# Kernel optimization log

Hardware: AMD Instinct MI355X
Metric: run time of the kernel (lower is better)

## Reference

```python
import jax, jax.numpy as jnp
import numpy as np

H = 16          # N_heads (Attention default)
DH = 32         # d per head (Attention default)
EPS = 1e-5      # torch LayerNorm eps
SCALE = float(1.0 / np.sqrt(DH))


def _ln(z, w, b):
    # LayerNorm over the last TWO dims (normalized_shape=(N_x, channel)), affine w/b of shape [2S, C]
    m = jnp.mean(z, axis=(-2, -1), keepdims=True)
    v = jnp.mean(jnp.square(z - m), axis=(-2, -1), keepdims=True)
    return (z - m) * jax.lax.rsqrt(v + EPS) * w + b


def _attention(a, p):
    # a: [2S, C]. Faithful to source: y = x.clone(), scores are NOT softmaxed (causal_mask=False).
    lx_w, lx_b, ly_w, ly_b, lf_w, lf_b, wq_w, wq_b, wk_w, wk_b, wv_w, wv_b, w1, b1, w2, b2, w3, b3 = p
    L = a.shape[0]
    xn = _ln(a, lx_w, lx_b)
    yn = _ln(a, ly_w, ly_b)
    q = (xn @ wq_w.T + wq_b).reshape(L, H, DH).transpose(1, 0, 2)  # [H, 2S, d]
    k = (yn @ wk_w.T + wk_b).reshape(L, H, DH).transpose(1, 0, 2)
    v = (yn @ wv_w.T + wv_b).reshape(L, H, DH).transpose(1, 0, 2)
    scores = jnp.einsum('hqd,hkd->hqk', q, k) * SCALE               # no softmax in source
    o = jnp.einsum('hqk,hkd->hqd', scores, v).transpose(1, 0, 2).reshape(L, H * DH)
    x1 = a + o @ w1.T + b1
    h = jax.nn.gelu(_ln(x1, lf_w, lf_b) @ w2.T + b2, approximate=False)
    return x1 + h @ w3.T + b3


def _forward(x, params):
    # x: [3, S, S, C]; params are stacked over the idx axis [S, ...] (one Attention per idx, shared across modes)
    S = x.shape[1]
    attn = jax.vmap(_attention, in_axes=(0, 0))
    for m1, m2 in [(0, 1), (2, 0), (1, 2)]:
        a = jnp.concatenate([x[m1], jnp.swapaxes(x[m2], 0, 1)], axis=1)  # [S, 2S, C]
        c = attn(a, params)                                              # [S, 2S, C]
        x = x.at[m1].set(c[:, :S, :])
        x = x.at[m2].set(c[:, S:, :])
    return x


def setup_inputs() -> dict:
    S, C, W = 16, 1024, 4
    D = H * DH   # 512
    L = 2 * S    # 32
    key = jax.random.key(0)
    ks = jax.random.split(key, 8)
    rn = lambda k, shp, s: jax.random.normal(k, shp, dtype=jnp.float32) * s
    return {
        'x': rn(ks[0], (3, S, S, C), 1.0),
        'lx_w': jnp.ones((S, L, C), jnp.float32), 'lx_b': jnp.zeros((S, L, C), jnp.float32),
        'ly_w': jnp.ones((S, L, C), jnp.float32), 'ly_b': jnp.zeros((S, L, C), jnp.float32),
        'lf_w': jnp.ones((S, L, C), jnp.float32), 'lf_b': jnp.zeros((S, L, C), jnp.float32),
        'wq_w': rn(ks[1], (S, D, C), 0.02), 'wq_b': jnp.zeros((S, D), jnp.float32),
        'wk_w': rn(ks[2], (S, D, C), 0.02), 'wk_b': jnp.zeros((S, D), jnp.float32),
        'wv_w': rn(ks[3], (S, D, C), 0.02), 'wv_b': jnp.zeros((S, D), jnp.float32),
        'w1': rn(ks[4], (S, C, D), 0.02), 'b1': jnp.zeros((S, C), jnp.float32),
        'w2': rn(ks[5], (S, W * C, C), 0.02), 'b2': jnp.zeros((S, W * C), jnp.float32),
        'w3': rn(ks[6], (S, C, W * C), 0.02), 'b3': jnp.zeros((S, C), jnp.float32),
    }


def reference(x, lx_w, lx_b, ly_w, ly_b, lf_w, lf_b, wq_w, wq_b, wk_w, wk_b, wv_w, wv_b, w1, b1, w2, b2, w3, b3):
    params = (lx_w, lx_b, ly_w, ly_b, lf_w, lf_b, wq_w, wq_b, wk_w, wk_b, wv_w, wv_b, w1, b1, w2, b2, w3, b3)
    return _forward(x, params)
```

## Files before the change

kernel.cpp:

```cpp
#include <hip/hip_runtime.h>


#define C1024 1024
#define D512  512
#define FF4096 4096
#define NELEM 32768.0f
#define EPSLN 1e-5f
#define QSCALE 0.17677669529663687f
#define LP 258

typedef __attribute__((ext_vector_type(8))) short bf16x8;
typedef __attribute__((ext_vector_type(4))) float f32x4;
typedef unsigned short u16;

__device__ inline u16 f2bf(float f) {
    unsigned u = __float_as_uint(f);
    u += 0x7fffu + ((u >> 16) & 1u);
    return (u16)(u >> 16);
}

__device__ inline bf16x8 cvt8(f32x4 a, f32x4 b) {
    bf16x8 r;
    r[0] = (short)f2bf(a[0]); r[1] = (short)f2bf(a[1]);
    r[2] = (short)f2bf(a[2]); r[3] = (short)f2bf(a[3]);
    r[4] = (short)f2bf(b[0]); r[5] = (short)f2bf(b[1]);
    r[6] = (short)f2bf(b[2]); r[7] = (short)f2bf(b[3]);
    return r;
}

struct Cvt6 {
    const float* s[6];
    u16* d[6];
    int N32[6], kzs[6], base[6];
};
__global__ void __launch_bounds__(256, 8) k_cvt6(Cvt6 a) {
    __shared__ float lds[16 * LP];
    int bid = blockIdx.x;
    int ts = 0;
#pragma unroll
    for (int j = 1; j < 6; ++j) if (bid >= a.base[j]) ts = j;
    int local = bid - a.base[ts];
    int kzs = a.kzs[ts], N32 = a.N32[ts];
    int kz = local % kzs;
    int b  = (local / kzs) & 1;
    int nt = (local / (kzs * 2)) % N32;
    int i  = local / (kzs * 2 * N32);
    int K = kzs * 256;
    int t = threadIdx.x;
    int row = t >> 4, c16 = t & 15;
    const float* Sp = a.s[ts] + ((size_t)((i * N32 + nt) * 32) + b * 16 + row) * K + kz * 256 + c16 * 4;
    float* Lrow = lds + row * LP + c16 * 4;
#pragma unroll
    for (int j = 0; j < 4; ++j) {
        f32x4 v = *(const f32x4*)(Sp + 64 * j);
        Lrow[64 * j]     = v[0];
        Lrow[64 * j + 1] = v[1];
        Lrow[64 * j + 2] = v[2];
        Lrow[64 * j + 3] = v[3];
    }
    __syncthreads();
    u16* Dp = a.d[ts] + (((size_t)(i * N32 + nt) * (kzs * 8) + kz * 8) * 1024) + b * 512;
#pragma unroll
    for (int p = 0; p < 2; ++p) {
        int u = p * 2048 + t * 8;
        int c   = u >> 9;
        int rem = u & 511;
        int kg = rem >> 7;
        int lr = (rem >> 3) & 15;
        const float* src = lds + lr * LP + c * 32 + kg * 8;
        f32x4 lo, hi;
        lo[0] = src[0]; lo[1] = src[1]; lo[2] = src[2]; lo[3] = src[3];
        hi[0] = src[4]; hi[1] = src[5]; hi[2] = src[6]; hi[3] = src[7];
        *(bf16x8*)(Dp + c * 1024 + rem) = cvt8(lo, hi);
    }
}

__device__ inline void mmz(const u16* __restrict__ act, const u16* __restrict__ p,
                           int nkk, f32x4& acc0, f32x4& acc1) {
#pragma unroll 4
    for (int j = 0; j < nkk; ++j) {
        bf16x8 aF = *(const bf16x8*)(act + j * 32);
        bf16x8 b0 = *(const bf16x8*)(p + (size_t)j * 1024);
        bf16x8 b1 = *(const bf16x8*)(p + (size_t)j * 1024 + 512);
        acc0 = __builtin_amdgcn_mfma_f32_16x16x32_bf16(aF, b0, acc0, 0, 0, 0);
        acc1 = __builtin_amdgcn_mfma_f32_16x16x32_bf16(aF, b1, acc1, 0, 0, 0);
    }
}

__device__ inline void reduce256(float& s, float& q, int t, float* lds) {
    for (int off = 32; off; off >>= 1) {
        s += __shfl_down(s, off, 64);
        q += __shfl_down(q, off, 64);
    }
    int wv = t >> 6;
    if ((t & 63) == 0) { lds[wv * 2] = s; lds[wv * 2 + 1] = q; }
    __syncthreads();
    if (t == 0) {
        lds[8] = lds[0] + lds[2] + lds[4] + lds[6];
        lds[9] = lds[1] + lds[3] + lds[5] + lds[7];
    }
    __syncthreads();
    s = lds[8]; q = lds[9];
}

__global__ void k_ln1(const float* __restrict__ s1, const float* __restrict__ s2,
                      const float* __restrict__ gw, const float* __restrict__ gb,
                      const float* __restrict__ hw, const float* __restrict__ hb,
                      float* __restrict__ a_buf,
                      u16* __restrict__ xn, u16* __restrict__ yn) {
    __shared__ float lds[10];
    int i = blockIdx.x, cb = blockIdx.y, t = threadIdx.x;
    float s = 0.f, q = 0.f;
#pragma unroll 4
    for (int rr = 0; rr < 32; ++rr) {
        const float* src = (rr < 16)
            ? (s1 + ((i * 16 + rr) << 10))
            : (s2 + (((rr - 16) * 16 + i) << 10));
        f32x4 v = *(const f32x4*)(src + t * 4);
        s += v[0] + v[1] + v[2] + v[3];
        q += v[0]*v[0] + v[1]*v[1] + v[2]*v[2] + v[3]*v[3];
        if ((t >> 5) == cb)
            *(f32x4*)(a_buf + ((i * 32 + rr) << 10) + t * 4) = v;
    }
    reduce256(s, q, t, lds);
    float mean = s * (1.f / NELEM);
    float var = q * (1.f / NELEM) - mean * mean;
    float inv = rsqrtf(var + EPSLN);
    int c = cb * 128 + (t & 31) * 4;
    int r0 = (t >> 5) * 4;
#pragma unroll
    for (int rr = 0; rr < 4; ++rr) {
        int row = r0 + rr;
        const float* src = (row < 16)
            ? (s1 + ((i * 16 + row) << 10))
            : (s2 + (((row - 16) * 16 + i) << 10));
        f32x4 v = *(const f32x4*)(src + c);
        int base = ((i * 32 + row) << 10) + c;
        f32x4 gwv = *(const f32x4*)(gw + base);
        f32x4 gbv = *(const f32x4*)(gb + base);
        f32x4 hwv = *(const f32x4*)(hw + base);
        f32x4 hbv = *(const f32x4*)(hb + base);
        float z0 = (v[0]-mean)*inv, z1 = (v[1]-mean)*inv, z2 = (v[2]-mean)*inv, z3 = (v[3]-mean)*inv;
        uint2 a, b;
        a.x = (unsigned)f2bf(z0*gwv[0]+gbv[0]) | ((unsigned)f2bf(z1*gwv[1]+gbv[1]) << 16);
        a.y = (unsigned)f2bf(z2*gwv[2]+gbv[2]) | ((unsigned)f2bf(z3*gwv[3]+gbv[3]) << 16);
        b.x = (unsigned)f2bf(z0*hwv[0]+hbv[0]) | ((unsigned)f2bf(z1*hwv[1]+hbv[1]) << 16);
        b.y = (unsigned)f2bf(z2*hwv[2]+hbv[2]) | ((unsigned)f2bf(z3*hwv[3]+hbv[3]) << 16);
        *(uint2*)(xn + base) = a;
        *(uint2*)(yn + base) = b;
    }
}

__global__ void k_ln2(const float* __restrict__ x1,
                      const float* __restrict__ gw, const float* __restrict__ gb,
                      u16* __restrict__ out) {
    __shared__ float lds[10];
    int i = blockIdx.x, cb = blockIdx.y, t = threadIdx.x;
    float s = 0.f, q = 0.f;
#pragma unroll 4
    for (int rr = 0; rr < 32; ++rr) {
        f32x4 v = *(const f32x4*)(x1 + ((i * 32 + rr) << 10) + t * 4);
        s += v[0] + v[1] + v[2] + v[3];
        q += v[0]*v[0] + v[1]*v[1] + v[2]*v[2] + v[3]*v[3];
    }
    reduce256(s, q, t, lds);
    float mean = s * (1.f / NELEM);
    float var = q * (1.f / NELEM) - mean * mean;
    float inv = rsqrtf(var + EPSLN);
    int c = cb * 128 + (t & 31) * 4;
    int r0 = (t >> 5) * 4;
#pragma unroll
    for (int rr = 0; rr < 4; ++rr) {
        int base = ((i * 32 + r0 + rr) << 10) + c;
        f32x4 v  = *(const f32x4*)(x1 + base);
        f32x4 gwv = *(const f32x4*)(gw + base);
        f32x4 gbv = *(const f32x4*)(gb + base);
        float z0 = (v[0]-mean)*inv, z1 = (v[1]-mean)*inv, z2 = (v[2]-mean)*inv, z3 = (v[3]-mean)*inv;
        uint2 a;
        a.x = (unsigned)f2bf(z0*gwv[0]+gbv[0]) | ((unsigned)f2bf(z1*gwv[1]+gbv[1]) << 16);
        a.y = (unsigned)f2bf(z2*gwv[2]+gbv[2]) | ((unsigned)f2bf(z3*gwv[3]+gbv[3]) << 16);
        *(uint2*)(out + base) = a;
    }
}

__global__ void __launch_bounds__(512, 4)
k_gemm_qkv(const u16* __restrict__ xn, const u16* __restrict__ yn,
           const u16* __restrict__ wq, const float* __restrict__ wqb,
           const u16* __restrict__ wk, const float* __restrict__ wkb,
           const u16* __restrict__ wv, const float* __restrict__ wvb,
           u16* __restrict__ qo, u16* __restrict__ ko, u16* __restrict__ vT) {
    __shared__ float Pl[2][32][64];
    int bx = blockIdx.x, i = blockIdx.y;
    int w = threadIdx.x >> 6, lane = threadIdx.x & 63;
    int kh = w >> 2, mh = (w >> 1) & 1, wn = w & 1;
    int lr = lane & 15, kg = lane >> 4;
    int sel = bx >> 3;
    int ntl = (bx - sel * 8) * 2 + wn;
    const u16* act = (sel == 0 ? xn : yn) + (i * 32 + mh * 16 + lr) * C1024 + kh * 512 + kg * 8;
    const u16* Wm = (sel == 0 ? wq : (sel == 1 ? wk : wv));
    const u16* p = Wm + (((size_t)i * 16 + ntl) * 32 + kh * 16) * 1024 + lane * 8;
    f32x4 a0 = {0.f, 0.f, 0.f, 0.f}, a1 = {0.f, 0.f, 0.f, 0.f};
    mmz(act, p, 16, a0, a1);
    int m0 = mh * 16 + kg * 4;
#pragma unroll
    for (int r = 0; r < 4; ++r) {
        Pl[kh][m0 + r][wn * 32 + lr] = a0[r];
        Pl[kh][m0 + r][wn * 32 + 16 + lr] = a1[r];
    }
    __syncthreads();
    int t = threadIdx.x;
    int row = t >> 4, c0 = (t & 15) * 4;
    int nloc = bx * 64 - sel * 512 + c0;
    const float* bias = (sel == 0 ? wqb : (sel == 1 ? wkb : wvb)) + i * D512 + nloc;
    float v0 = Pl[0][row][c0]     + Pl[1][row][c0]     + bias[0];
    float v1 = Pl[0][row][c0 + 1] + Pl[1][row][c0 + 1] + bias[1];
    float v2 = Pl[0][row][c0 + 2] + Pl[1][row][c0 + 2] + bias[2];
    float v3 = Pl[0][row][c0 + 3] + Pl[1][row][c0 + 3] + bias[3];
    if (sel == 0) {
        uint2 a;
        a.x = (unsigned)f2bf(v0 * QSCALE) | ((unsigned)f2bf(v1 * QSCALE) << 16);
        a.y = (unsigned)f2bf(v2 * QSCALE) | ((unsigned)f2bf(v3 * QSCALE) << 16);
        *(uint2*)(qo + (i * 32 + row) * D512 + nloc) = a;
    } else if (sel == 1) {
        uint2 a;
        a.x = (unsigned)f2bf(v0) | ((unsigned)f2bf(v1) << 16);
        a.y = (unsigned)f2bf(v2) | ((unsigned)f2bf(v3) << 16);
        *(uint2*)(ko + (i * 32 + row) * D512 + nloc) = a;
    } else {
        int h = nloc >> 5, d = nloc & 31;
        u16* vb = vT + ((i * 16 + h) * 32 + d) * 32 + row;
        vb[0]  = f2bf(v0);
        vb[32] = f2bf(v1);
        vb[64] = f2bf(v2);
        vb[96] = f2bf(v3);
    }
}

__global__ void k_attn(const u16* __restrict__ q, const u16* __restrict__ k,
                       const u16* __restrict__ vT, u16* __restrict__ o) {
    __shared__ __align__(16) u16 Sm[4][32][32];
    int i = blockIdx.x;
    int w = threadIdx.x >> 6, lane = threadIdx.x & 63;
    int h = blockIdx.y * 4 + w;
    int lr = lane & 15, kg = lane >> 4;
    const u16* qb = q + i * 32 * D512 + h * 32 + kg * 8;
    const u16* kb = k + i * 32 * D512 + h * 32 + kg * 8;
    bf16x8 a0 = *(const bf16x8*)(qb + lr * D512);
    bf16x8 a1 = *(const bf16x8*)(qb + (16 + lr) * D512);
    bf16x8 b0 = *(const bf16x8*)(kb + lr * D512);
    bf16x8 b1 = *(const bf16x8*)(kb + (16 + lr) * D512);
    f32x4 z = {0.f, 0.f, 0.f, 0.f};
    f32x4 s00 = __builtin_amdgcn_mfma_f32_16x16x32_bf16(a0, b0, z, 0, 0, 0);
    f32x4 s01 = __builtin_amdgcn_mfma_f32_16x16x32_bf16(a0, b1, z, 0, 0, 0);
    f32x4 s10 = __builtin_amdgcn_mfma_f32_16x16x32_bf16(a1, b0, z, 0, 0, 0);
    f32x4 s11 = __builtin_amdgcn_mfma_f32_16x16x32_bf16(a1, b1, z, 0, 0, 0);
    int mr = kg * 4;
#pragma unroll
    for (int r = 0; r < 4; ++r) {
        Sm[w][mr + r][lr]           = f2bf(s00[r]);
        Sm[w][mr + r][16 + lr]      = f2bf(s01[r]);
        Sm[w][16 + mr + r][lr]      = f2bf(s10[r]);
        Sm[w][16 + mr + r][16 + lr] = f2bf(s11[r]);
    }
    __syncthreads();
    bf16x8 p0 = *(const bf16x8*)&Sm[w][lr][kg * 8];
    bf16x8 p1 = *(const bf16x8*)&Sm[w][16 + lr][kg * 8];
    const u16* vb = vT + (i * 16 + h) * 32 * 32 + kg * 8;
    bf16x8 v0 = *(const bf16x8*)(vb + lr * 32);
    bf16x8 v1 = *(const bf16x8*)(vb + (16 + lr) * 32);
    f32x4 o00 = __builtin_amdgcn_mfma_f32_16x16x32_bf16(p0, v0, z, 0, 0, 0);
    f32x4 o01 = __builtin_amdgcn_mfma_f32_16x16x32_bf16(p0, v1, z, 0, 0, 0);
    f32x4 o10 = __builtin_amdgcn_mfma_f32_16x16x32_bf16(p1, v0, z, 0, 0, 0);
    f32x4 o11 = __builtin_amdgcn_mfma_f32_16x16x32_bf16(p1, v1, z, 0, 0, 0);
#pragma unroll
    for (int r = 0; r < 4; ++r) {
        o[(i * 32 + mr + r) * D512 + h * 32 + lr]           = f2bf(o00[r]);
        o[(i * 32 + mr + r) * D512 + h * 32 + 16 + lr]      = f2bf(o01[r]);
        o[(i * 32 + 16 + mr + r) * D512 + h * 32 + lr]      = f2bf(o10[r]);
        o[(i * 32 + 16 + mr + r) * D512 + h * 32 + 16 + lr] = f2bf(o11[r]);
    }
}

__global__ void __launch_bounds__(512, 4)
k_gemm_w1(const u16* __restrict__ ob, const u16* __restrict__ W,
          const float* __restrict__ bias, const float* __restrict__ a_buf,
          float* __restrict__ x1) {
    __shared__ float Pl[2][32][64];
    int bx = blockIdx.x, i = blockIdx.y;
    int w = threadIdx.x >> 6, lane = threadIdx.x & 63;
    int kh = w >> 2, mh = (w >> 1) & 1, wn = w & 1;
    int lr = lane & 15, kg = lane >> 4;
    int nt = bx * 2 + wn;
    const u16* act = ob + (i * 32 + mh * 16 + lr) * D512 + kh * 256 + kg * 8;
    const u16* p = W + (((size_t)i * 32 + nt) * 16 + kh * 8) * 1024 + lane * 8;
    f32x4 a0 = {0.f, 0.f, 0.f, 0.f}, a1 = {0.f, 0.f, 0.f, 0.f};
    mmz(act, p, 8, a0, a1);
    int m0 = mh * 16 + kg * 4;
#pragma unroll
    for (int r = 0; r < 4; ++r) {
        Pl[kh][m0 + r][wn * 32 + lr] = a0[r];
        Pl[kh][m0 + r][wn * 32 + 16 + lr] = a1[r];
    }
    __syncthreads();
    int t = threadIdx.x;
    int row = t >> 4, c0 = (t & 15) * 4;
    int n = bx * 64 + c0;
    int base = ((i * 32 + row) << 10) + n;
    f32x4 bv = *(const f32x4*)(bias + i * C1024 + n);
    f32x4 av = *(const f32x4*)(a_buf + base);
    f32x4 r;
    r[0] = Pl[0][row][c0]     + Pl[1][row][c0]     + bv[0] + av[0];
    r[1] = Pl[0][row][c0 + 1] + Pl[1][row][c0 + 1] + bv[1] + av[1];
    r[2] = Pl[0][row][c0 + 2] + Pl[1][row][c0 + 2] + bv[2] + av[2];
    r[3] = Pl[0][row][c0 + 3] + Pl[1][row][c0 + 3] + bv[3] + av[3];
    *(f32x4*)(x1 + base) = r;
}

__global__ void __launch_bounds__(256, 4)
k_gemm_w2(const u16* __restrict__ lnf, const u16* __restrict__ W,
          const float* __restrict__ bias, u16* __restrict__ hb) {
    int bx = blockIdx.x, i = blockIdx.y;
    int w = threadIdx.x >> 6, lane = threadIdx.x & 63;
    int mh = w & 1, wn = w >> 1, lr = lane & 15, kg = lane >> 4;
    int nt = bx * 2 + wn;
    const u16* act = lnf + (i * 32 + mh * 16 + lr) * C1024 + kg * 8;
    const u16* p = W + (((size_t)i * 128 + nt) * 32) * 1024 + lane * 8;
    f32x4 a0 = {0.f, 0.f, 0.f, 0.f}, a1 = {0.f, 0.f, 0.f, 0.f};
    mmz(act, p, 32, a0, a1);
    int m0 = mh * 16 + kg * 4;
    int nb = bx * 64 + wn * 32;
    int n0 = nb + lr, n1 = nb + 16 + lr;
    float b0 = bias[i * FF4096 + n0], b1 = bias[i * FF4096 + n1];
#pragma unroll
    for (int r = 0; r < 4; ++r) {
        float t0 = a0[r] + b0;
        float t1 = a1[r] + b1;
        float g0 = 0.5f * t0 * (1.f + erff(t0 * 0.70710678118654752f));
        float g1 = 0.5f * t1 * (1.f + erff(t1 * 0.70710678118654752f));
        hb[(i * 32 + m0 + r) * FF4096 + n0] = f2bf(g0);
        hb[(i * 32 + m0 + r) * FF4096 + n1] = f2bf(g1);
    }
}

__global__ void __launch_bounds__(1024, 4)
k_gemm_w3(const u16* __restrict__ hb, const u16* __restrict__ W,
          const float* __restrict__ bias, const float* __restrict__ x1,
          float* __restrict__ xout, int m1, int m2) {
    __shared__ float Pl[4][32][64];
    int bx = blockIdx.x, i = blockIdx.y;
    int w = threadIdx.x >> 6, lane = threadIdx.x & 63;
    int kq = w >> 2, mh = (w >> 1) & 1, wn = w & 1;
    int lr = lane & 15, kg = lane >> 4;
    int nt = bx * 2 + wn;
    const u16* act = hb + (i * 32 + mh * 16 + lr) * FF4096 + kq * 1024 + kg * 8;
    const u16* p = W + (((size_t)i * 32 + nt) * 128 + kq * 32) * 1024 + lane * 8;
    f32x4 a0 = {0.f, 0.f, 0.f, 0.f}, a1 = {0.f, 0.f, 0.f, 0.f};
    mmz(act, p, 32, a0, a1);
    int m0 = mh * 16 + kg * 4;
#pragma unroll
    for (int r = 0; r < 4; ++r) {
        Pl[kq][m0 + r][wn * 32 + lr] = a0[r];
        Pl[kq][m0 + r][wn * 32 + 16 + lr] = a1[r];
    }
    __syncthreads();
    int t = threadIdx.x;
    int row = t >> 5, c0 = (t & 31) * 2;
    int n = bx * 64 + c0;
    int dst = (row < 16) ? (((m1 * 16 + i) * 16 + row) << 10)
                         : (((m2 * 16 + i) * 16 + (row - 16)) << 10);
    int base = ((i * 32 + row) << 10) + n;
#pragma unroll
    for (int j = 0; j < 2; ++j) {
        float v = Pl[0][row][c0 + j] + Pl[1][row][c0 + j]
                + Pl[2][row][c0 + j] + Pl[3][row][c0 + j]
                + bias[i * C1024 + n + j] + x1[base + j];
        xout[dst + n + j] = v;
    }
}

extern "C" void kernel_launch(void* const* d_in, const int* in_sizes, int n_in,
                              void* d_out, int out_size, void* d_ws, size_t ws_size,
                              hipStream_t stream) {
    const float* x_in = (const float*)d_in[0];
    const float* lx_w = (const float*)d_in[1];
    const float* lx_b = (const float*)d_in[2];
    const float* ly_w = (const float*)d_in[3];
    const float* ly_b = (const float*)d_in[4];
    const float* lf_w = (const float*)d_in[5];
    const float* lf_b = (const float*)d_in[6];
    const float* wq_w = (const float*)d_in[7];
    const float* wq_b = (const float*)d_in[8];
    const float* wk_w = (const float*)d_in[9];
    const float* wk_b = (const float*)d_in[10];
    const float* wv_w = (const float*)d_in[11];
    const float* wv_b = (const float*)d_in[12];
    const float* w1   = (const float*)d_in[13];
    const float* b1   = (const float*)d_in[14];
    const float* w2   = (const float*)d_in[15];
    const float* b2   = (const float*)d_in[16];
    const float* w3   = (const float*)d_in[17];
    const float* b3   = (const float*)d_in[18];

    float* xbuf = (float*)d_out;
    char* ws = (char*)d_ws;
    float* a_buf  = (float*)(ws);
    float* x1_buf = (float*)(ws + (2u << 20));
    u16*   xn     = (u16*)(ws + (4u << 20));
    u16*   yn     = (u16*)(ws + (5u << 20));
    u16*   lnf    = (u16*)(ws + (6u << 20));
    u16*   qb     = (u16*)(ws + (7u << 20));
    u16*   kb     = (u16*)(ws + 7 * (1u << 20) + (1u << 19));
    u16*   vT     = (u16*)(ws + (8u << 20));
    u16*   ob     = (u16*)(ws + 8 * (1u << 20) + (1u << 19));
    u16*   hbuf   = (u16*)(ws + (9u << 20));
    u16*   wq16   = (u16*)(ws + (16u  << 20));
    u16*   wk16   = (u16*)(ws + (32u  << 20));
    u16*   wv16   = (u16*)(ws + (48u  << 20));
    u16*   w1_16  = (u16*)(ws + (64u  << 20));
    u16*   w2_16  = (u16*)(ws + (80u  << 20));
    u16*   w3_16  = (u16*)(ws + (208u << 20));

    Cvt6 ca;
    ca.s[0] = wq_w; ca.d[0] = wq16;  ca.N32[0] = 16;  ca.kzs[0] = 4;  ca.base[0] = 0;
    ca.s[1] = wk_w; ca.d[1] = wk16;  ca.N32[1] = 16;  ca.kzs[1] = 4;  ca.base[1] = 2048;
    ca.s[2] = wv_w; ca.d[2] = wv16;  ca.N32[2] = 16;  ca.kzs[2] = 4;  ca.base[2] = 4096;
    ca.s[3] = w1;   ca.d[3] = w1_16; ca.N32[3] = 32;  ca.kzs[3] = 2;  ca.base[3] = 6144;
    ca.s[4] = w2;   ca.d[4] = w2_16; ca.N32[4] = 128; ca.kzs[4] = 4;  ca.base[4] = 8192;
    ca.s[5] = w3;   ca.d[5] = w3_16; ca.N32[5] = 32;  ca.kzs[5] = 16; ca.base[5] = 24576;
    k_cvt6<<<40960, 256, 0, stream>>>(ca);

    const size_t SLAB = (size_t)16 * 16 * 1024;
    const int modes[3][2] = {{0, 1}, {2, 0}, {1, 2}};
    for (int mi = 0; mi < 3; ++mi) {
        int m1 = modes[mi][0], m2 = modes[mi][1];
        const float* s1 = (mi == 2) ? (xbuf + m1 * SLAB) : (x_in + m1 * SLAB);
        const float* s2 = (mi == 0) ? (x_in + m2 * SLAB) : (xbuf + m2 * SLAB);
        k_ln1<<<dim3(16, 8), 256, 0, stream>>>(s1, s2, lx_w, lx_b, ly_w, ly_b, a_buf, xn, yn);
        k_gemm_qkv<<<dim3(24, 16), 512, 0, stream>>>(xn, yn, wq16, wq_b, wk16, wk_b, wv16, wv_b, qb, kb, vT);
        k_attn<<<dim3(16, 4), 256, 0, stream>>>(qb, kb, vT, ob);
        k_gemm_w1<<<dim3(16, 16), 512, 0, stream>>>(ob, w1_16, b1, a_buf, x1_buf);
        k_ln2<<<dim3(16, 8), 256, 0, stream>>>(x1_buf, lf_w, lf_b, lnf);
        k_gemm_w2<<<dim3(64, 16), 256, 0, stream>>>(lnf, w2_16, b2, hbuf);
        k_gemm_w3<<<dim3(16, 16), 1024, 0, stream>>>(hbuf, w3_16, b3, x1_buf, xbuf, m1, m2);
    }
}
```

Baseline: 536.5 us.

## Fuse w2/w3 fp32-to-bf16 conversion into the first-mode FFN GEMMs

```diff
diff --git a/kernel.cpp b/kernel.cpp
--- a/kernel.cpp
+++ b/kernel.cpp
@@ -28,17 +28,17 @@
     return r;
 }
 
-struct Cvt6 {
-    const float* s[6];
-    u16* d[6];
-    int N32[6], kzs[6], base[6];
+struct Cvt4 {
+    const float* s[4];
+    u16* d[4];
+    int N32[4], kzs[4], base[4];
 };
-__global__ void __launch_bounds__(256, 8) k_cvt6(Cvt6 a) {
+__global__ void __launch_bounds__(256, 8) k_cvt6(Cvt4 a) {
     __shared__ float lds[16 * LP];
     int bid = blockIdx.x;
     int ts = 0;
 #pragma unroll
-    for (int j = 1; j < 6; ++j) if (bid >= a.base[j]) ts = j;
+    for (int j = 1; j < 4; ++j) if (bid >= a.base[j]) ts = j;
     int local = bid - a.base[ts];
     int kzs = a.kzs[ts], N32 = a.N32[ts];
     int kz = local % kzs;
@@ -72,6 +72,85 @@
         lo[0] = src[0]; lo[1] = src[1]; lo[2] = src[2]; lo[3] = src[3];
         hi[0] = src[4]; hi[1] = src[5]; hi[2] = src[6]; hi[3] = src[7];
         *(bf16x8*)(Dp + c * 1024 + rem) = cvt8(lo, hi);
+    }
+}
+
+template<int EPI>
+__global__ void __launch_bounds__(256, 4)
+k_cvtgemm(const float* __restrict__ W32, u16* __restrict__ W16,
+          const u16* __restrict__ act, int kzs, int N32,
+          const float* __restrict__ bias,
+          u16* __restrict__ hb,
+          const float* __restrict__ x1, float* __restrict__ xout,
+          int m1, int m2) {
+    __shared__ float lds[16 * LP];
+    __shared__ float Pl[4][32][16];
+    int bx = blockIdx.x, i = blockIdx.y;
+    int b = bx & 1, nt = bx >> 1;
+    int K = kzs * 256;
+    int t = threadIdx.x;
+    int w = t >> 6, lane = t & 63;
+    int lr = lane & 15, kg = lane >> 4;
+    int row = t >> 4, c16 = t & 15;
+    const float* Sp = W32 + ((size_t)(i * N32 + nt) * 32 + b * 16 + row) * K + c16 * 4;
+    u16* Dbase = W16 + ((size_t)(i * N32 + nt) * (kzs * 8)) * 1024 + b * 512;
+    const u16* A0 = act + ((size_t)(i * 32) + lr) * K + kg * 8;
+    const u16* A1 = A0 + (size_t)16 * K;
+    f32x4 acc0 = {0.f, 0.f, 0.f, 0.f}, acc1 = {0.f, 0.f, 0.f, 0.f};
+    float* Lrow = lds + row * LP + c16 * 4;
+    const float* src = lds + lr * LP + kg * 8;
+    for (int kz = 0; kz < kzs; ++kz) {
+        const float* Sk = Sp + kz * 256;
+#pragma unroll
+        for (int j = 0; j < 4; ++j) {
+            f32x4 v = *(const f32x4*)(Sk + 64 * j);
+            Lrow[64 * j]     = v[0];
+            Lrow[64 * j + 1] = v[1];
+            Lrow[64 * j + 2] = v[2];
+            Lrow[64 * j + 3] = v[3];
+        }
+        __syncthreads();
+        u16* Dp = Dbase + (size_t)(kz * 8) * 1024;
+#pragma unroll
+        for (int p = 0; p < 2; ++p) {
+            int c = p * 4 + w;
+            const float* s8 = src + c * 32;
+            f32x4 lo, hi;
+            lo[0] = s8[0]; lo[1] = s8[1]; lo[2] = s8[2]; lo[3] = s8[3];
+            hi[0] = s8[4]; hi[1] = s8[5]; hi[2] = s8[6]; hi[3] = s8[7];
+            bf16x8 r = cvt8(lo, hi);
+            *(bf16x8*)(Dp + c * 1024 + lane * 8) = r;
+            int kk = kz * 8 + c;
+            bf16x8 aF0 = *(const bf16x8*)(A0 + kk * 32);
+            bf16x8 aF1 = *(const bf16x8*)(A1 + kk * 32);
+            acc0 = __builtin_amdgcn_mfma_f32_16x16x32_bf16(aF0, r, acc0, 0, 0, 0);
+            acc1 = __builtin_amdgcn_mfma_f32_16x16x32_bf16(aF1, r, acc1, 0, 0, 0);
+        }
+        __syncthreads();
+    }
+#pragma unroll
+    for (int rr = 0; rr < 4; ++rr) {
+        Pl[w][kg * 4 + rr][lr]      = acc0[rr];
+        Pl[w][16 + kg * 4 + rr][lr] = acc1[rr];
+    }
+    __syncthreads();
+    int m = t >> 3, nl0 = (t & 7) * 2;
+#pragma unroll
+    for (int jj = 0; jj < 2; ++jj) {
+        int nl = nl0 + jj;
+        float v = Pl[0][m][nl] + Pl[1][m][nl] + Pl[2][m][nl] + Pl[3][m][nl];
+        int n = nt * 32 + b * 16 + nl;
+        if constexpr (EPI == 0) {
+            float tt = v + bias[i * FF4096 + n];
+            float g = 0.5f * tt * (1.f + erff(tt * 0.70710678118654752f));
+            hb[((size_t)(i * 32) + m) * FF4096 + n] = f2bf(g);
+        } else {
+            int base = ((i * 32 + m) << 10) + n;
+            float vv = v + bias[i * C1024 + n] + x1[base];
+            int dst = (m < 16) ? (((m1 * 16 + i) * 16 + m) << 10)
+                               : (((m2 * 16 + i) * 16 + (m - 16)) << 10);
+            xout[dst + n] = vv;
+        }
     }
 }
 
@@ -420,14 +499,12 @@
     u16*   w2_16  = (u16*)(ws + (80u  << 20));
     u16*   w3_16  = (u16*)(ws + (208u << 20));
 
-    Cvt6 ca;
+    Cvt4 ca;
     ca.s[0] = wq_w; ca.d[0] = wq16;  ca.N32[0] = 16;  ca.kzs[0] = 4;  ca.base[0] = 0;
     ca.s[1] = wk_w; ca.d[1] = wk16;  ca.N32[1] = 16;  ca.kzs[1] = 4;  ca.base[1] = 2048;
     ca.s[2] = wv_w; ca.d[2] = wv16;  ca.N32[2] = 16;  ca.kzs[2] = 4;  ca.base[2] = 4096;
     ca.s[3] = w1;   ca.d[3] = w1_16; ca.N32[3] = 32;  ca.kzs[3] = 2;  ca.base[3] = 6144;
-    ca.s[4] = w2;   ca.d[4] = w2_16; ca.N32[4] = 128; ca.kzs[4] = 4;  ca.base[4] = 8192;
-    ca.s[5] = w3;   ca.d[5] = w3_16; ca.N32[5] = 32;  ca.kzs[5] = 16; ca.base[5] = 24576;
-    k_cvt6<<<40960, 256, 0, stream>>>(ca);
+    k_cvt6<<<8192, 256, 0, stream>>>(ca);
 
     const size_t SLAB = (size_t)16 * 16 * 1024;
     const int modes[3][2] = {{0, 1}, {2, 0}, {1, 2}};
@@ -440,7 +517,14 @@
         k_attn<<<dim3(16, 4), 256, 0, stream>>>(qb, kb, vT, ob);
         k_gemm_w1<<<dim3(16, 16), 512, 0, stream>>>(ob, w1_16, b1, a_buf, x1_buf);
         k_ln2<<<dim3(16, 8), 256, 0, stream>>>(x1_buf, lf_w, lf_b, lnf);
-        k_gemm_w2<<<dim3(64, 16), 256, 0, stream>>>(lnf, w2_16, b2, hbuf);
-        k_gemm_w3<<<dim3(16, 16), 1024, 0, stream>>>(hbuf, w3_16, b3, x1_buf, xbuf, m1, m2);
-    }
-}
+        if (mi == 0) {
+            k_cvtgemm<0><<<dim3(256, 16), 256, 0, stream>>>(
+                w2, w2_16, lnf, 4, 128, b2, hbuf, nullptr, nullptr, 0, 0);
+            k_cvtgemm<1><<<dim3(64, 16), 256, 0, stream>>>(
+                w3, w3_16, hbuf, 16, 32, b3, nullptr, x1_buf, xbuf, m1, m2);
+        } else {
+            k_gemm_w2<<<dim3(64, 16), 256, 0, stream>>>(lnf, w2_16, b2, hbuf);
+            k_gemm_w3<<<dim3(16, 16), 1024, 0, stream>>>(hbuf, w3_16, b3, x1_buf, xbuf, m1, m2);
+        }
+    }
+}
```

Result: faster. 507.5 us (-5.4%).
